# Kernel optimization log

Measured on AMD Instinct MI355X. Metric: run time of the kernel, lower is better.

## Reference

```python
import jax, jax.numpy as jnp
import numpy as np

S = 2        # subsample_rate
EPS = 1e-5   # BatchNorm eps


def maxpool(x, k):
    B, C, H, W = x.shape
    return x.reshape(B, C, H // k, k, W // k, k).max(axis=(3, 5))


def conv1x1(x, w, b):
    # x: [B,C,H,W], w: [O,C], b: [O]
    return jnp.einsum('bchw,oc->bohw', x, w) + b[None, :, None, None]


def upsample_bilinear_ac(y, s):
    # torch nn.Upsample(mode='bilinear', scale_factor=s, align_corners=True)
    B, C, h, w = y.shape
    H, W = h * s, w * s
    ri = jnp.arange(H, dtype=jnp.float32) * ((h - 1) / (H - 1))
    ci = jnp.arange(W, dtype=jnp.float32) * ((w - 1) / (W - 1))
    r0 = jnp.floor(ri).astype(jnp.int32); r1 = jnp.minimum(r0 + 1, h - 1)
    c0 = jnp.floor(ci).astype(jnp.int32); c1 = jnp.minimum(c0 + 1, w - 1)
    wr = (ri - r0)[None, None, :, None]
    wc = (ci - c0)[None, None, None, :]
    top = y[:, :, r0, :] * (1.0 - wr) + y[:, :, r1, :] * wr
    return top[:, :, :, c0] * (1.0 - wc) + top[:, :, :, c1] * wc


def setup_inputs() -> dict:
    key = jax.random.key(0)
    ks = jax.random.split(key, 12)
    B, C, IC, H, W = 4, 256, 128, 192, 192
    sc = 0.05  # keep attention logits in a sane range
    x = jax.random.normal(ks[0], (B, C, H, W), jnp.float32)
    g_w = jax.random.normal(ks[1], (IC, C), jnp.float32) * sc
    g_b = jax.random.normal(ks[2], (IC,), jnp.float32) * sc
    theta_w = jax.random.normal(ks[3], (IC, C), jnp.float32) * sc
    theta_b = jax.random.normal(ks[4], (IC,), jnp.float32) * sc
    phi_w = jax.random.normal(ks[5], (IC, C), jnp.float32) * sc
    phi_b = jax.random.normal(ks[6], (IC,), jnp.float32) * sc
    W_w = jax.random.normal(ks[7], (C, IC, 3, 3), jnp.float32) * sc
    W_b = jax.random.normal(ks[8], (C,), jnp.float32) * sc
    bn_gamma = jnp.ones((C,), jnp.float32)
    bn_beta = jnp.zeros((C,), jnp.float32)
    bn_mean = jax.random.normal(ks[9], (C,), jnp.float32) * sc
    bn_var = jax.random.uniform(ks[10], (C,), jnp.float32) + 0.5
    return dict(x=x, g_w=g_w, g_b=g_b, theta_w=theta_w, theta_b=theta_b,
                phi_w=phi_w, phi_b=phi_b, W_w=W_w, W_b=W_b,
                bn_gamma=bn_gamma, bn_beta=bn_beta, bn_mean=bn_mean, bn_var=bn_var)


def reference(x, g_w, g_b, theta_w, theta_b, phi_w, phi_b, W_w, W_b,
              bn_gamma, bn_beta, bn_mean, bn_var):
    B, C, H, Wd = x.shape
    IC = g_w.shape[0]
    xp = maxpool(x, S)                               # [B,C,H/S,W/S]
    theta = conv1x1(xp, theta_w, theta_b)            # [B,IC,h,w]
    g = maxpool(conv1x1(xp, g_w, g_b), 2)            # [B,IC,h/2,w/2]
    phi = maxpool(conv1x1(xp, phi_w, phi_b), 2)      # [B,IC,h/2,w/2]
    h, w = theta.shape[2], theta.shape[3]
    th = theta.reshape(B, IC, h * w).transpose(0, 2, 1)   # [B,Nt,IC]
    ph = phi.reshape(B, IC, -1)                           # [B,IC,Np]
    gx = g.reshape(B, IC, -1).transpose(0, 2, 1)          # [B,Np,IC]
    f = jnp.einsum('bnc,bcm->bnm', th, ph)                # [B,Nt,Np]
    a = jax.nn.softmax(f, axis=-1)
    y = jnp.einsum('bnm,bmc->bnc', a, gx)                 # [B,Nt,IC]
    y = y.transpose(0, 2, 1).reshape(B, IC, h, w)
    y = upsample_bilinear_ac(y, S)                        # [B,IC,H,W]
    wy = jax.lax.conv_general_dilated(
        y, W_w, (1, 1), ((1, 1), (1, 1)),
        dimension_numbers=('NCHW', 'OIHW', 'NCHW')) + W_b[None, :, None, None]
    inv = bn_gamma / jnp.sqrt(bn_var + EPS)
    wy = (wy - bn_mean[None, :, None, None]) * inv[None, :, None, None] + bn_beta[None, :, None, None]
    return (wy + x, wy)
```

## Files before the change

### kernel.cpp

```cpp
#include <hip/hip_runtime.h>
#include <hip/hip_bf16.h>
#include <math.h>

#define B_   4
#define C_   256
#define ICH  128
#define H_   192
#define W_   192
#define hs   96
#define ws2  96
#define HW   (hs*ws2)
#define HP   48
#define WP   48
#define NP   (HP*WP)
#define EPSB 1e-5f
#define PADW 194
#define TOT  ((size_t)B_*C_*H_*W_)

#define QB 64
#define KB 64
#define NT (NP/KB)
#define SM_OFF 20.0f

using bf16x8 = __attribute__((ext_vector_type(8))) short;
using f32x4  = __attribute__((ext_vector_type(4))) float;
using f32x16 = __attribute__((ext_vector_type(16))) float;

#define OFF_XPB   ((size_t)0)
#define OFF_THB   ((size_t)4718592)
#define OFF_PHB   ((size_t)7077888)
#define OFF_GBT   ((size_t)7667712)
#define OFF_WB3   ((size_t)8257536)
#define OFF_Y96N  ((size_t)8306688)
#define OFF_ST    ((size_t)13025280)
#define OFF_WT    ((size_t)13025792)
#define OFF_YPAD  ((size_t)13173248)

static __device__ __forceinline__ float b2f(unsigned short u) {
  union { unsigned int i; float f; } c; c.i = (unsigned int)u << 16; return c.f;
}

__global__ __launch_bounds__(256) void k_pool_nhwc(const float* __restrict__ x,
                                                   __hip_bfloat16* __restrict__ xpb) {
  int idx = blockIdx.x * 256 + threadIdx.x;
  int cg = idx & 31;
  int n  = (idx >> 5) % HW;
  int b  = idx / (32 * HW);
  int pi = n / ws2, pj = n % ws2;
  const float* xb = x + (((size_t)b * C_ + cg * 8) * H_ + 2 * pi) * W_ + 2 * pj;
  union { ushort u[8]; uint4 v; } pk;
#pragma unroll
  for (int cc = 0; cc < 8; ++cc) {
    const float* s = xb + (size_t)cc * H_ * W_;
    float v = fmaxf(fmaxf(s[0], s[1]), fmaxf(s[W_], s[W_ + 1]));
    __hip_bfloat16 hv = __float2bfloat16(v);
    pk.u[cc] = *(ushort*)&hv;
  }
  *(uint4*)(xpb + ((size_t)b * HW + n) * C_ + cg * 8) = pk.v;
}

__global__ __launch_bounds__(256) void k_wprep(const float* __restrict__ tw,
                                               const float* __restrict__ gw,
                                               const float* __restrict__ pw,
                                               __hip_bfloat16* __restrict__ wb3) {
  int idx = blockIdx.x * 256 + threadIdx.x;
  int set = idx >> 15; int rem = idx & 32767;
  const float* src = set == 0 ? tw : (set == 1 ? gw : pw);
  wb3[idx] = __float2bfloat16(src[rem]);
}

__global__ __launch_bounds__(256, 3) void k_qkv(
    const __hip_bfloat16* __restrict__ xpb,
    const __hip_bfloat16* __restrict__ wb3,
    const float* __restrict__ tb, const float* __restrict__ gb_,
    const float* __restrict__ pb_,
    __hip_bfloat16* __restrict__ thb,
    __hip_bfloat16* __restrict__ gbt,
    __hip_bfloat16* __restrict__ phb) {
  __shared__ __align__(16) char ldsX[2][192 * 128];
  int t = threadIdx.x;
  int lane = t & 63, li = lane & 15, g4 = lane >> 4;
  int wid = t >> 6;
  int wave_o = wid >> 1, wave_n = wid & 1;
  int i   = blockIdx.x;
  int set = blockIdx.y;
  int b   = blockIdx.z;
  const __hip_bfloat16* wset = wb3 + (size_t)set * 128 * 256;
  const float* bias = set == 0 ? tb : (set == 1 ? gb_ : pb_);
  const size_t xbase = (size_t)b * HW * C_;

  f32x4 acc[4][6];
#pragma unroll
  for (int fo = 0; fo < 4; ++fo)
#pragma unroll
    for (int fq = 0; fq < 6; ++fq) acc[fo][fq] = (f32x4){0.f, 0.f, 0.f, 0.f};

#define STAGEX(step, buf)                                                      \
  for (int e = t; e < 192 * 8; e += 256) {                                     \
    int j = e >> 3, ch = e & 7;                                                \
    int pix = (2 * i + (j & 1)) * ws2 + (j >> 1);                              \
    *(uint4*)(ldsX[buf] + j * 128 + ((ch * 16) ^ ((j & 7) << 4))) =            \
        *(const uint4*)(xpb + xbase + (size_t)pix * C_ + (step) * 64 + ch * 8);\
  }

  STAGEX(0, 0)
  __syncthreads();
  for (int step = 0; step < 4; ++step) {
    int buf = step & 1;
    if (step < 3) { STAGEX(step + 1, buf ^ 1) }
    bf16x8 af[4][2];
#pragma unroll
    for (int fo = 0; fo < 4; ++fo)
#pragma unroll
      for (int ks = 0; ks < 2; ++ks) {
        int o = wave_o * 64 + fo * 16 + li;
        af[fo][ks] = *(const bf16x8*)(wset + (size_t)o * C_ + step * 64 + ks * 32 + g4 * 8);
      }
#pragma unroll
    for (int ks = 0; ks < 2; ++ks)
#pragma unroll
      for (int fq = 0; fq < 6; ++fq) {
        int j = wave_n * 96 + fq * 16 + li;
        bf16x8 bx = *(const bf16x8*)(ldsX[buf] + j * 128 + ((ks * 64 + g4 * 16) ^ ((j & 7) << 4)));
#pragma unroll
        for (int fo = 0; fo < 4; ++fo)
          acc[fo][fq] = __builtin_amdgcn_mfma_f32_16x16x32_bf16(af[fo][ks], bx, acc[fo][fq], 0, 0, 0);
      }
    __syncthreads();
  }

  if (set == 0) {
#pragma unroll
    for (int fo = 0; fo < 4; ++fo) {
      int ob = wave_o * 64 + fo * 16 + g4 * 4;
#pragma unroll
      for (int fq = 0; fq < 6; ++fq) {
        int j = wave_n * 96 + fq * 16 + li;
        int pix = (2 * i + (j & 1)) * ws2 + (j >> 1);
        union { ushort u[4]; uint2 v; } pk;
#pragma unroll
        for (int r = 0; r < 4; ++r) {
          __hip_bfloat16 hv = __float2bfloat16(acc[fo][fq][r] + bias[ob + r]);
          pk.u[r] = *(ushort*)&hv;
        }
        *(uint2*)(thb + ((size_t)b * HW + pix) * ICH + ob) = pk.v;
      }
    }
  } else {
#pragma unroll
    for (int fo = 0; fo < 4; ++fo) {
      int ob = wave_o * 64 + fo * 16 + g4 * 4;
#pragma unroll
      for (int fq = 0; fq < 6; ++fq) {
        float pv[4];
#pragma unroll
        for (int r = 0; r < 4; ++r) {
          float p = acc[fo][fq][r];
          p = fmaxf(p, __shfl_xor(p, 1, 64));
          p = fmaxf(p, __shfl_xor(p, 2, 64));
          pv[r] = p;
        }
        if ((li & 3) == 0) {
          int pc = wave_n * 24 + fq * 4 + (li >> 2);
          int pp = i * WP + pc;
          if (set == 1) {
#pragma unroll
            for (int r = 0; r < 4; ++r)
              gbt[((size_t)b * ICH + ob + r) * NP + pp] = __float2bfloat16(pv[r] + bias[ob + r]);
          } else {
            union { ushort u[4]; uint2 v; } pk;
#pragma unroll
            for (int r = 0; r < 4; ++r) {
              __hip_bfloat16 hv = __float2bfloat16(pv[r] + bias[ob + r]);
              pk.u[r] = *(ushort*)&hv;
            }
            *(uint2*)(phb + ((size_t)b * NP + pp) * ICH + ob) = pk.v;
          }
        }
      }
    }
  }
}

__global__ __launch_bounds__(256) void k_attn_mfma(
    const __hip_bfloat16* __restrict__ thb,
    const __hip_bfloat16* __restrict__ phb,
    const __hip_bfloat16* __restrict__ gbt,
    __hip_bfloat16* __restrict__ y96b) {
  __shared__ __align__(16) char Kl[KB * 256];
  __shared__ __align__(16) char Vl[ICH * KB * 2];
  __shared__ __align__(16) char Pl[4][16 * KB * 2];
  int t = threadIdx.x;
  int lane = t & 63, li = lane & 15, g = lane >> 4;
  int w = t >> 6;
  int flat = blockIdx.x;
  int swz = (flat & 7) * 72 + (flat >> 3);
  int b  = swz / 144;
  int q0 = (swz % 144) * QB;

  bf16x8 aq[4];
  {
    const __hip_bfloat16* qp = thb + ((size_t)b * HW + q0 + w * 16 + li) * ICH + g * 8;
#pragma unroll
    for (int ks = 0; ks < 4; ++ks) aq[ks] = *(const bf16x8*)(qp + ks * 32);
  }

  f32x4 acc_o[8];
#pragma unroll
  for (int ct = 0; ct < 8; ++ct) acc_o[ct] = (f32x4){0.f, 0.f, 0.f, 0.f};
  float l_acc[4] = {0.f, 0.f, 0.f, 0.f};

  char* Pw = (char*)Pl[w];

  for (int kt = 0; kt < NT; ++kt) {
    int m0 = kt * KB;
    __syncthreads();
    for (int e = t; e < KB * 16; e += 256) {
      int mm = e >> 4, ch = e & 15;
      *(uint4*)(Kl + mm * 256 + ((ch * 16) ^ ((mm & 7) << 4))) =
          *(const uint4*)(phb + ((size_t)b * NP + m0 + mm) * ICH + ch * 8);
    }
    for (int e = t; e < ICH * 8; e += 256) {
      int c = e >> 3, ch = e & 7;
      *(uint4*)(Vl + c * 128 + ((ch * 16) ^ ((c & 7) << 4))) =
          *(const uint4*)(gbt + ((size_t)b * ICH + c) * NP + m0 + ch * 8);
    }
    __syncthreads();

    f32x4 s[4];
#pragma unroll
    for (int mt = 0; mt < 4; ++mt) s[mt] = (f32x4){0.f, 0.f, 0.f, 0.f};
#pragma unroll
    for (int mt = 0; mt < 4; ++mt) {
      int m = mt * 16 + li;
#pragma unroll
      for (int ks = 0; ks < 4; ++ks) {
        bf16x8 bk = *(const bf16x8*)(Kl + m * 256 + ((ks * 64 + g * 16) ^ ((li & 7) << 4)));
        s[mt] = __builtin_amdgcn_mfma_f32_16x16x32_bf16(aq[ks], bk, s[mt], 0, 0, 0);
      }
    }

#pragma unroll
    for (int mt = 0; mt < 4; ++mt) {
#pragma unroll
      for (int r = 0; r < 4; ++r) {
        float p = __expf(s[mt][r] - SM_OFF);
        s[mt][r] = p;
        l_acc[r] += p;
      }
    }

#pragma unroll
    for (int mt = 0; mt < 4; ++mt) {
      int m = mt * 16 + li;
#pragma unroll
      for (int r = 0; r < 4; ++r) {
        int ql = g * 4 + r;
        __hip_bfloat16 hv = __float2bfloat16(s[mt][r]);
        *(ushort*)(Pw + ql * 128 + ((m * 2) ^ ((ql & 7) << 4))) = *(ushort*)&hv;
      }
    }

    bf16x8 pa[2];
#pragma unroll
    for (int ks = 0; ks < 2; ++ks)
      pa[ks] = *(const bf16x8*)(Pw + li * 128 + ((ks * 64 + g * 16) ^ ((li & 7) << 4)));
#pragma unroll
    for (int ct = 0; ct < 8; ++ct) {
      int c = ct * 16 + li;
#pragma unroll
      for (int ks = 0; ks < 2; ++ks) {
        bf16x8 bv = *(const bf16x8*)(Vl + c * 128 + ((ks * 64 + g * 16) ^ ((c & 7) << 4)));
        acc_o[ct] = __builtin_amdgcn_mfma_f32_16x16x32_bf16(pa[ks], bv, acc_o[ct], 0, 0, 0);
      }
    }
  }

  float inv[4];
#pragma unroll
  for (int r = 0; r < 4; ++r) {
    float l = l_acc[r];
    l += __shfl_xor(l, 1, 64);
    l += __shfl_xor(l, 2, 64);
    l += __shfl_xor(l, 4, 64);
    l += __shfl_xor(l, 8, 64);
    inv[r] = 1.f / l;
  }
  __hip_bfloat16* ob = y96b + ((size_t)b * HW + q0 + w * 16 + g * 4) * ICH + li;
#pragma unroll
  for (int r = 0; r < 4; ++r)
#pragma unroll
    for (int ct = 0; ct < 8; ++ct)
      ob[(size_t)r * ICH + ct * 16] = __float2bfloat16(acc_o[ct][r] * inv[r]);
}

__global__ __launch_bounds__(256) void k_up_pad(const __hip_bfloat16* __restrict__ y96b,
                                                __hip_bfloat16* __restrict__ ypad) {
  int idx = blockIdx.x * 256 + threadIdx.x;
  int icb  = idx & 15;
  int rest = idx >> 4;
  int pc = rest % PADW;
  int rest2 = rest / PADW;
  int pr = rest2 % PADW;
  int b  = rest2 / PADW;
  __hip_bfloat16* dst = ypad + ((size_t)(b * PADW + pr) * PADW + pc) * ICH + icb * 8;
  if (pr == 0 || pr == PADW - 1 || pc == 0 || pc == PADW - 1) {
    uint4 z = {0, 0, 0, 0};
    *(uint4*)dst = z;
    return;
  }
  int p = pr - 1, q = pc - 1;
  const float sc = 95.0f / 191.0f;
  float ri = p * sc, ci = q * sc;
  int r0 = (int)ri; int r1 = min(r0 + 1, hs - 1); float wr = ri - r0;
  int c0 = (int)ci; int c1 = min(c0 + 1, ws2 - 1); float wc = ci - c0;
  const __hip_bfloat16* base = y96b + (size_t)b * HW * ICH + icb * 8;
  union { ushort u[8]; uint4 v; } a, bb, cc, dd, pk;
  a.v  = *(const uint4*)(base + ((size_t)r0 * ws2 + c0) * ICH);
  bb.v = *(const uint4*)(base + ((size_t)r0 * ws2 + c1) * ICH);
  cc.v = *(const uint4*)(base + ((size_t)r1 * ws2 + c0) * ICH);
  dd.v = *(const uint4*)(base + ((size_t)r1 * ws2 + c1) * ICH);
#pragma unroll
  for (int j = 0; j < 8; ++j) {
    float top = b2f(a.u[j]) * (1.f - wr) + b2f(cc.u[j]) * wr;
    float bot = b2f(bb.u[j]) * (1.f - wr) + b2f(dd.u[j]) * wr;
    float v = top * (1.f - wc) + bot * wc;
    __hip_bfloat16 hv = __float2bfloat16(v);
    pk.u[j] = *(ushort*)&hv;
  }
  *(uint4*)dst = pk.v;
}

__global__ __launch_bounds__(256) void k_wt(const float* __restrict__ Ww,
                                            __hip_bfloat16* __restrict__ Wt) {
  int idx = blockIdx.x * 256 + threadIdx.x;
  int ic  = idx & 127;
  int o   = (idx >> 7) & 255;
  int tap = idx >> 15;
  Wt[idx] = __float2bfloat16(Ww[(size_t)o * (ICH * 9) + ic * 9 + tap]);
}

__global__ __launch_bounds__(256) void k_bnprep(const float* __restrict__ Wb,
                                                const float* __restrict__ bg,
                                                const float* __restrict__ bb,
                                                const float* __restrict__ bm,
                                                const float* __restrict__ bv,
                                                float* __restrict__ ST) {
  int o = threadIdx.x;
  float sc = bg[o] * rsqrtf(bv[o] + EPSB);
  ST[o] = sc;
  ST[256 + o] = (Wb[o] - bm[o]) * sc + bb[o];
}

#define ABY 12288
#define BBY 6208
#define BUF (ABY + BBY)
__global__ __launch_bounds__(256) void k_conv3_mfma(
    const __hip_bfloat16* __restrict__ ypad,
    const __hip_bfloat16* __restrict__ Wt,
    const float* __restrict__ ST,
    const float* __restrict__ x,
    float* __restrict__ out) {
  __shared__ __align__(16) char ldsM[2 * BUF];
  int t = threadIdx.x;
  int lane = t & 63;
  int l31 = lane & 31, h = lane >> 5;
  int wid = t >> 6;
  int wave_o = wid >> 1, wave_q = wid & 1;

  int flat = blockIdx.x;
  int swz = (flat & 7) * 192 + (flat >> 3);
  int p  = swz % H_;
  int zz = swz / H_;
  int b  = zz >> 1;
  int o0 = (zz & 1) * 128;

  f32x16 acc[2][3];
#pragma unroll
  for (int i = 0; i < 2; ++i)
#pragma unroll
    for (int j = 0; j < 3; ++j)
#pragma unroll
      for (int r = 0; r < 16; ++r) acc[i][j][r] = 0.f;

  const size_t ypbase = (size_t)b * PADW * PADW * ICH;

#define STG(s_, buf_)                                                           \
  {                                                                             \
    int kh_ = (s_) >> 3, icE_ = (s_) & 7;                                       \
    char* base_ = ldsM + (buf_) * BUF;                                          \
    const __hip_bfloat16* wb_ = Wt + ((size_t)(kh_ * 3) * 256 + o0) * ICH + icE_ * 16; \
    _Pragma("unroll")                                                           \
    for (int rr = 0; rr < 3; ++rr) {                                            \
      int e = rr * 256 + t;                                                     \
      int tap_ = e >> 8, ch_ = (e >> 7) & 1, o_ = e & 127;                      \
      __builtin_amdgcn_global_load_lds(                                         \
          (const __attribute__((address_space(1))) void*)(wb_ + ((size_t)tap_ * 256 + o_) * ICH + ch_ * 8), \
          (__attribute__((address_space(3))) void*)(base_ + (rr * 256 + (t & 192)) * 16), \
          16, 0, 0);                                                            \
    }                                                                           \
    const __hip_bfloat16* br_ = ypad + ypbase + (size_t)(p + kh_) * PADW * ICH + icE_ * 16; \
    _Pragma("unroll")                                                           \
    for (int rr = 0; rr < 2; ++rr) {                                            \
      int e = rr * 256 + t;                                                     \
      if (e < 388) {                                                            \
        int ch_ = (e >= 194) ? 1 : 0;                                           \
        int col_ = e - ch_ * 194;                                               \
        __builtin_amdgcn_global_load_lds(                                       \
            (const __attribute__((address_space(1))) void*)(br_ + (size_t)col_ * ICH + ch_ * 8), \
            (__attribute__((address_space(3))) void*)(base_ + ABY + (rr * 256 + (t & 192)) * 16), \
            16, 0, 0);                                                          \
      }                                                                         \
    }                                                                           \
  }

  STG(0, 0)
  __syncthreads();
  for (int s = 0; s < 24; ++s) {
    if (s < 23) { STG(s + 1, (s + 1) & 1) }
    const char* Ab = ldsM + (s & 1) * BUF;
    const char* Bb = Ab + ABY;
#pragma unroll
    for (int kw = 0; kw < 3; ++kw) {
      bf16x8 afr[2], bfr[3];
#pragma unroll
      for (int fo = 0; fo < 2; ++fo)
        afr[fo] = *(const bf16x8*)(Ab + (kw * 256 + h * 128 + wave_o * 64 + fo * 32 + l31) * 16);
#pragma unroll
      for (int fq = 0; fq < 3; ++fq)
        bfr[fq] = *(const bf16x8*)(Bb + (h * 194 + wave_q * 96 + fq * 32 + l31 + kw) * 16);
#pragma unroll
      for (int fo = 0; fo < 2; ++fo)
#pragma unroll
        for (int fq = 0; fq < 3; ++fq)
          acc[fo][fq] = __builtin_amdgcn_mfma_f32_32x32x16_bf16(
              afr[fo], bfr[fq], acc[fo][fq], 0, 0, 0);
    }
    __syncthreads();
  }

#pragma unroll
  for (int fo = 0; fo < 2; ++fo) {
#pragma unroll
    for (int fq = 0; fq < 3; ++fq) {
#pragma unroll
      for (int r = 0; r < 16; ++r) {
        int o = o0 + wave_o * 64 + fo * 32 + (r & 3) + 8 * (r >> 2) + 4 * h;
        int q = wave_q * 96 + fq * 32 + l31;
        size_t oi = (((size_t)b * C_ + o) * H_ + p) * W_ + q;
        float val = acc[fo][fq][r] * ST[o] + ST[256 + o];
        out[TOT + oi] = val;
        out[oi] = val + x[oi];
      }
    }
  }
}

extern "C" void kernel_launch(void* const* d_in, const int* in_sizes, int n_in,
                              void* d_out, int out_size, void* d_ws, size_t ws_size,
                              hipStream_t stream) {
  const float* x    = (const float*)d_in[0];
  const float* g_w  = (const float*)d_in[1];
  const float* g_b  = (const float*)d_in[2];
  const float* th_w = (const float*)d_in[3];
  const float* th_b = (const float*)d_in[4];
  const float* ph_w = (const float*)d_in[5];
  const float* ph_b = (const float*)d_in[6];
  const float* W_w  = (const float*)d_in[7];
  const float* W_b  = (const float*)d_in[8];
  const float* bn_g = (const float*)d_in[9];
  const float* bn_b = (const float*)d_in[10];
  const float* bn_m = (const float*)d_in[11];
  const float* bn_v = (const float*)d_in[12];
  float* out = (float*)d_out;
  float* ws  = (float*)d_ws;

  __hip_bfloat16* xpb = (__hip_bfloat16*)(ws + OFF_XPB);
  __hip_bfloat16* thb = (__hip_bfloat16*)(ws + OFF_THB);
  __hip_bfloat16* phb = (__hip_bfloat16*)(ws + OFF_PHB);
  __hip_bfloat16* gbt = (__hip_bfloat16*)(ws + OFF_GBT);
  __hip_bfloat16* wb3 = (__hip_bfloat16*)(ws + OFF_WB3);
  __hip_bfloat16* y96b = (__hip_bfloat16*)(ws + OFF_Y96N);
  float* ST   = ws + OFF_ST;
  __hip_bfloat16* Wt   = (__hip_bfloat16*)(ws + OFF_WT);
  __hip_bfloat16* ypad = (__hip_bfloat16*)(ws + OFF_YPAD);

  k_pool_nhwc<<<(B_ * HW * 32) / 256, 256, 0, stream>>>(x, xpb);
  k_wprep<<<(3 * 128 * 256) / 256, 256, 0, stream>>>(th_w, g_w, ph_w, wb3);
  k_qkv<<<dim3(HP, 3, B_), 256, 0, stream>>>(xpb, wb3, th_b, g_b, ph_b, thb, gbt, phb);
  k_attn_mfma<<<dim3(B_ * (HW / QB)), 256, 0, stream>>>(thb, phb, gbt, y96b);
  k_up_pad<<<(B_ * PADW * PADW * 16) / 256, 256, 0, stream>>>(y96b, ypad);
  k_wt<<<(9 * 256 * 128) / 256, 256, 0, stream>>>(W_w, Wt);
  k_bnprep<<<1, 256, 0, stream>>>(W_b, bn_g, bn_b, bn_m, bn_v, ST);
  k_conv3_mfma<<<dim3(H_ * B_ * 2), 256, 0, stream>>>(ypad, Wt, ST, x, out);
}
```

Before: 461.5 us.

## Re-layout padded activation and conv weights into channel-chunk-major blocks for contiguous staging

The padded upsampled activation and the transposed 3x3 weights are re-laid out so that each 8-channel chunk forms its own plane, indexed [b][row][ic8][col][8] and [tap][ic8][o][8]. The conv kernel's global-to-LDS staging loads then read contiguous 16-byte runs across columns and output channels instead of strided 256-byte rows. The conv kernel also gets a launch-bounds occupancy hint of 3 blocks per CU. The up-pad kernel now does its loads and stores as pairs of 8-byte accesses, which may cost some access efficiency, and the occupancy hint may cause register spills.

```diff
diff --git a/kernel.cpp b/kernel.cpp
--- a/kernel.cpp
+++ b/kernel.cpp
@@ -297,16 +297,17 @@
 __global__ __launch_bounds__(256) void k_up_pad(const __hip_bfloat16* __restrict__ y96b,
                                                 __hip_bfloat16* __restrict__ ypad) {
   int idx = blockIdx.x * 256 + threadIdx.x;
-  int icb  = idx & 15;
-  int rest = idx >> 4;
-  int pc = rest % PADW;
-  int rest2 = rest / PADW;
-  int pr = rest2 % PADW;
-  int b  = rest2 / PADW;
-  __hip_bfloat16* dst = ypad + ((size_t)(b * PADW + pr) * PADW + pc) * ICH + icb * 8;
+  int pc  = idx % PADW;
+  int r2  = idx / PADW;
+  int ic8 = r2 & 15;
+  int r3  = r2 >> 4;
+  int pr  = r3 % PADW;
+  int b   = r3 / PADW;
+  __hip_bfloat16* dst = ypad + (size_t)idx * 8;
   if (pr == 0 || pr == PADW - 1 || pc == 0 || pc == PADW - 1) {
-    uint4 z = {0, 0, 0, 0};
-    *(uint4*)dst = z;
+    uint2 z = {0, 0};
+    *(uint2*)dst = z;
+    *(uint2*)(dst + 4) = z;
     return;
   }
   int p = pr - 1, q = pc - 1;
@@ -314,29 +315,42 @@
   float ri = p * sc, ci = q * sc;
   int r0 = (int)ri; int r1 = min(r0 + 1, hs - 1); float wr = ri - r0;
   int c0 = (int)ci; int c1 = min(c0 + 1, ws2 - 1); float wc = ci - c0;
-  const __hip_bfloat16* base = y96b + (size_t)b * HW * ICH + icb * 8;
-  union { ushort u[8]; uint4 v; } a, bb, cc, dd, pk;
-  a.v  = *(const uint4*)(base + ((size_t)r0 * ws2 + c0) * ICH);
-  bb.v = *(const uint4*)(base + ((size_t)r0 * ws2 + c1) * ICH);
-  cc.v = *(const uint4*)(base + ((size_t)r1 * ws2 + c0) * ICH);
-  dd.v = *(const uint4*)(base + ((size_t)r1 * ws2 + c1) * ICH);
-#pragma unroll
-  for (int j = 0; j < 8; ++j) {
+  const __hip_bfloat16* base = y96b + (size_t)b * HW * ICH + ic8 * 8;
+  union { ushort u[4]; uint2 v; } a, bb, cc, dd, pk;
+  a.v  = *(const uint2*)(base + ((size_t)r0 * ws2 + c0) * ICH);
+  bb.v = *(const uint2*)(base + ((size_t)r0 * ws2 + c1) * ICH);
+  cc.v = *(const uint2*)(base + ((size_t)r1 * ws2 + c0) * ICH);
+  dd.v = *(const uint2*)(base + ((size_t)r1 * ws2 + c1) * ICH);
+  union { ushort u[4]; uint2 v; } a2, bb2, cc2, dd2, pk2;
+  a2.v  = *(const uint2*)(base + ((size_t)r0 * ws2 + c0) * ICH + 4);
+  bb2.v = *(const uint2*)(base + ((size_t)r0 * ws2 + c1) * ICH + 4);
+  cc2.v = *(const uint2*)(base + ((size_t)r1 * ws2 + c0) * ICH + 4);
+  dd2.v = *(const uint2*)(base + ((size_t)r1 * ws2 + c1) * ICH + 4);
+#pragma unroll
+  for (int j = 0; j < 4; ++j) {
     float top = b2f(a.u[j]) * (1.f - wr) + b2f(cc.u[j]) * wr;
     float bot = b2f(bb.u[j]) * (1.f - wr) + b2f(dd.u[j]) * wr;
     float v = top * (1.f - wc) + bot * wc;
     __hip_bfloat16 hv = __float2bfloat16(v);
     pk.u[j] = *(ushort*)&hv;
-  }
-  *(uint4*)dst = pk.v;
+    float top2 = b2f(a2.u[j]) * (1.f - wr) + b2f(cc2.u[j]) * wr;
+    float bot2 = b2f(bb2.u[j]) * (1.f - wr) + b2f(dd2.u[j]) * wr;
+    float v2 = top2 * (1.f - wc) + bot2 * wc;
+    __hip_bfloat16 hv2 = __float2bfloat16(v2);
+    pk2.u[j] = *(ushort*)&hv2;
+  }
+  *(uint2*)dst = pk.v;
+  *(uint2*)(dst + 4) = pk2.v;
 }
 
 __global__ __launch_bounds__(256) void k_wt(const float* __restrict__ Ww,
                                             __hip_bfloat16* __restrict__ Wt) {
   int idx = blockIdx.x * 256 + threadIdx.x;
-  int ic  = idx & 127;
-  int o   = (idx >> 7) & 255;
+  int lo  = idx & 7;
+  int o   = (idx >> 3) & 255;
+  int ic8 = (idx >> 11) & 15;
   int tap = idx >> 15;
+  int ic  = ic8 * 8 + lo;
   Wt[idx] = __float2bfloat16(Ww[(size_t)o * (ICH * 9) + ic * 9 + tap]);
 }
 
@@ -355,7 +369,7 @@
 #define ABY 12288
 #define BBY 6208
 #define BUF (ABY + BBY)
-__global__ __launch_bounds__(256) void k_conv3_mfma(
+__global__ __launch_bounds__(256, 3) void k_conv3_mfma(
     const __hip_bfloat16* __restrict__ ypad,
     const __hip_bfloat16* __restrict__ Wt,
     const float* __restrict__ ST,
@@ -383,31 +397,31 @@
 #pragma unroll
       for (int r = 0; r < 16; ++r) acc[i][j][r] = 0.f;
 
-  const size_t ypbase = (size_t)b * PADW * PADW * ICH;
-
 #define STG(s_, buf_)                                                           \
   {                                                                             \
     int kh_ = (s_) >> 3, icE_ = (s_) & 7;                                       \
     char* base_ = ldsM + (buf_) * BUF;                                          \
-    const __hip_bfloat16* wb_ = Wt + ((size_t)(kh_ * 3) * 256 + o0) * ICH + icE_ * 16; \
+    const __hip_bfloat16* wb_ = Wt;                                             \
     _Pragma("unroll")                                                           \
     for (int rr = 0; rr < 3; ++rr) {                                            \
       int e = rr * 256 + t;                                                     \
       int tap_ = e >> 8, ch_ = (e >> 7) & 1, o_ = e & 127;                      \
+      size_t gsl = (((size_t)(kh_ * 3 + tap_) * 16 + icE_ * 2 + ch_) * 256 + o0 + o_) * 8; \
       __builtin_amdgcn_global_load_lds(                                         \
-          (const __attribute__((address_space(1))) void*)(wb_ + ((size_t)tap_ * 256 + o_) * ICH + ch_ * 8), \
+          (const __attribute__((address_space(1))) void*)(wb_ + gsl),           \
           (__attribute__((address_space(3))) void*)(base_ + (rr * 256 + (t & 192)) * 16), \
           16, 0, 0);                                                            \
     }                                                                           \
-    const __hip_bfloat16* br_ = ypad + ypbase + (size_t)(p + kh_) * PADW * ICH + icE_ * 16; \
+    const __hip_bfloat16* br_ = ypad;                                           \
     _Pragma("unroll")                                                           \
     for (int rr = 0; rr < 2; ++rr) {                                            \
       int e = rr * 256 + t;                                                     \
       if (e < 388) {                                                            \
         int ch_ = (e >= 194) ? 1 : 0;                                           \
         int col_ = e - ch_ * 194;                                               \
+        size_t gsl = (((size_t)(b * PADW + p + kh_) * 16 + icE_ * 2 + ch_) * PADW + col_) * 8; \
         __builtin_amdgcn_global_load_lds(                                       \
-            (const __attribute__((address_space(1))) void*)(br_ + (size_t)col_ * ICH + ch_ * 8), \
+            (const __attribute__((address_space(1))) void*)(br_ + gsl),         \
             (__attribute__((address_space(3))) void*)(base_ + ABY + (rr * 256 + (t & 192)) * 16), \
             16, 0, 0);                                                          \
       }                                                                         \
@@ -489,8 +503,8 @@
   k_wprep<<<(3 * 128 * 256) / 256, 256, 0, stream>>>(th_w, g_w, ph_w, wb3);
   k_qkv<<<dim3(HP, 3, B_), 256, 0, stream>>>(xpb, wb3, th_b, g_b, ph_b, thb, gbt, phb);
   k_attn_mfma<<<dim3(B_ * (HW / QB)), 256, 0, stream>>>(thb, phb, gbt, y96b);
-  k_up_pad<<<(B_ * PADW * PADW * 16) / 256, 256, 0, stream>>>(y96b, ypad);
-  k_wt<<<(9 * 256 * 128) / 256, 256, 0, stream>>>(W_w, Wt);
+  k_up_pad<<<(B_ * PADW * 16 * PADW) / 256, 256, 0, stream>>>(y96b, ypad);
+  k_wt<<<(9 * 16 * 256 * 8) / 256, 256, 0, stream>>>(W_w, Wt);
   k_bnprep<<<1, 256, 0, stream>>>(W_b, bn_g, bn_b, bn_m, bn_v, ST);
   k_conv3_mfma<<<dim3(H_ * B_ * 2), 256, 0, stream>>>(ypad, Wt, ST, x, out);
 }
```

New measurement: 538.5 us. 1.17x slower.
